# Performance work log

Measured on AMD Instinct MI355X. Metric: run time of the kernel, lower is better.

## Reference

```python
import jax, jax.numpy as jnp
import numpy as np

INPUT_DIM = 512
OUTPUT_DIM = 512
NUM_BASIS = 16
GRID_MIN, GRID_MAX = -2.0, 2.0
LN_EPS = 1e-5


def rbf_basis(x):
    # x: [batch, input_dim] -> [batch, input_dim, num_basis]
    centers = jnp.linspace(GRID_MIN, GRID_MAX, NUM_BASIS, dtype=x.dtype)  # [K]
    h = (GRID_MAX - GRID_MIN) / (NUM_BASIS - 1)
    z = (x[..., None] - centers) / h
    return jnp.exp(-(z * z))


def setup_inputs() -> dict:
    key = jax.random.key(0)
    k1, k2, k3 = jax.random.split(key, 3)
    x = jax.random.normal(k1, (4096, INPUT_DIM), dtype=jnp.float32)
    weights = jax.random.normal(k2, (OUTPUT_DIM, INPUT_DIM, NUM_BASIS), dtype=jnp.float32) * 0.1
    base_weights = jax.random.normal(k3, (OUTPUT_DIM, INPUT_DIM), dtype=jnp.float32) * 0.1
    ln_gamma = jnp.ones((OUTPUT_DIM,), dtype=jnp.float32)
    ln_beta = jnp.zeros((OUTPUT_DIM,), dtype=jnp.float32)
    return {"x": x, "weights": weights, "base_weights": base_weights,
            "ln_gamma": ln_gamma, "ln_beta": ln_beta}


def reference(x, weights, base_weights, ln_gamma, ln_beta):
    # per-edge basis expansion: [B, I, K]
    basis = rbf_basis(x)
    # fused contraction replacing the nested python loops:
    # out[b, j] = sum_{i,k} basis[b, i, k] * weights[j, i, k]
    out = jnp.einsum('bik,jik->bj', basis, weights)
    # residual base activation path
    out = out + jax.nn.silu(x) @ base_weights.T
    # layer norm over output_dim
    mean = jnp.mean(out, axis=-1, keepdims=True)
    var = jnp.var(out, axis=-1, keepdims=True)
    out = (out - mean) * jax.lax.rsqrt(var + LN_EPS) * ln_gamma + ln_beta
    return out
```

## Files before the change

### kernel.cpp

```cpp
#include <hip/hip_runtime.h>
#include <hip/hip_bf16.h>


typedef __bf16 bf16x8 __attribute__((ext_vector_type(8)));
typedef __bf16 bf16x4 __attribute__((ext_vector_type(4)));
typedef float  f32x4  __attribute__((ext_vector_type(4)));

#define KT 8704
#define SPLITS 8
#define KS (KT / SPLITS)
#define NIT (KS / 32)
#define CPE (4096 * 512)
#define ABUF (256 * 32)

__device__ __forceinline__ void gll16(const __bf16* g, __bf16* l) {
    __builtin_amdgcn_global_load_lds(
        (const __attribute__((address_space(1))) void*)g,
        (__attribute__((address_space(3))) void*)l, 16, 0, 0);
}

__global__ void prep_AB(const float* __restrict__ x, const float* __restrict__ W,
                        const float* __restrict__ Wb, __bf16* __restrict__ A,
                        __bf16* __restrict__ B) {
    if (blockIdx.x < 8192) {
        int t = blockIdx.x * 256 + threadIdx.x;
        int b = t >> 9;
        int i = t & 511;
        float xv = x[t];
        float zb = 3.75f * xv + 7.5f;
        bf16x8 lo, hi;
#pragma unroll
        for (int k = 0; k < 8; ++k) { float z = zb - (float)k; lo[k]   = (__bf16)__expf(-z * z); }
#pragma unroll
        for (int k = 8; k < 16; ++k){ float z = zb - (float)k; hi[k-8] = (__bf16)__expf(-z * z); }
        size_t base = (size_t)b * KT + (size_t)i * 16;
        *(bf16x8*)(A + base)     = lo;
        *(bf16x8*)(A + base + 8) = hi;
        float s = xv / (1.0f + __expf(-xv));
        A[(size_t)b * KT + 8192 + i] = (__bf16)s;
    } else {
        int t = (blockIdx.x - 8192) * 256 + threadIdx.x;
        int j = t / 2176;
        int c = (t - j * 2176) * 4;
        float4 v;
        if (c < 8192) v = *(const float4*)&W[(size_t)j * 8192 + c];
        else          v = *(const float4*)&Wb[(size_t)j * 512 + (c - 8192)];
        bf16x4 o;
        o[0] = (__bf16)v.x; o[1] = (__bf16)v.y; o[2] = (__bf16)v.z; o[3] = (__bf16)v.w;
        *(bf16x4*)&B[(size_t)j * KT + c] = o;
    }
}

__global__ __launch_bounds__(512, 2) void gemm_bt(const __bf16* __restrict__ A,
                                                  const __bf16* __restrict__ B,
                                                  __bf16* __restrict__ Cp) {
    __shared__ __attribute__((aligned(16))) __bf16 As[3 * ABUF];
    __shared__ __attribute__((aligned(16))) __bf16 Bs[3 * ABUF];

    const int tid  = threadIdx.x;
    const int wave = tid >> 6, lane = tid & 63;
    const int q    = lane >> 4, r16 = lane & 15;
    const int m0 = blockIdx.x * 256, n0 = blockIdx.y * 256, k0 = blockIdx.z * KS;
    const int wm = wave >> 2, wn = wave & 3;

    const int srow = tid >> 2, sqk = (tid & 3) ^ ((srow >> 1) & 3);
    const __bf16* gA0 = A + (size_t)(m0 + srow) * KT + k0 + sqk * 8;
    const __bf16* gA1 = A + (size_t)(m0 + srow + 128) * KT + k0 + sqk * 8;
    const __bf16* gB0 = B + (size_t)(n0 + srow) * KT + k0 + sqk * 8;
    const __bf16* gB1 = B + (size_t)(n0 + srow + 128) * KT + k0 + sqk * 8;

    f32x4 acc[8][4] = {};

    const int qa    = q ^ ((r16 >> 1) & 3);
    const int awOff = (wm * 128 + r16) * 32 + qa * 8;
    const int bwOff = (wn * 64  + r16) * 32 + qa * 8;

    auto stage = [&](int t, int sb) {
        const int ko = t * 32;
        const int so = sb * ABUF;
        gll16(gA0 + ko, &As[so + tid * 8]);
        gll16(gA1 + ko, &As[so + (tid + 512) * 8]);
        gll16(gB0 + ko, &Bs[so + tid * 8]);
        gll16(gB1 + ko, &Bs[so + (tid + 512) * 8]);
    };

    auto compute = [&](int cb) {
        const __bf16* Aw = &As[cb * ABUF + awOff];
        const __bf16* Bw = &Bs[cb * ABUF + bwOff];
        bf16x8 af[8], bg[4];
#pragma unroll
        for (int mi = 0; mi < 8; ++mi) af[mi] = *(const bf16x8*)(Aw + mi * 512);
#pragma unroll
        for (int ni = 0; ni < 4; ++ni) bg[ni] = *(const bf16x8*)(Bw + ni * 512);
        __builtin_amdgcn_s_setprio(1);
#pragma unroll
        for (int mi = 0; mi < 8; ++mi)
#pragma unroll
            for (int ni = 0; ni < 4; ++ni)
                acc[mi][ni] = __builtin_amdgcn_mfma_f32_16x16x32_bf16(
                    af[mi], bg[ni], acc[mi][ni], 0, 0, 0);
        __builtin_amdgcn_s_setprio(0);
    };

    stage(0, 0);
    stage(1, 1);
    asm volatile("s_waitcnt vmcnt(4)" ::: "memory");
    __builtin_amdgcn_s_barrier();

    int cb = 0;
    for (int it = 0; it < NIT - 1; ++it) {
        int sb = cb - 1; if (sb < 0) sb = 2;
        stage(it + 2, sb);
        compute(cb);
        asm volatile("s_waitcnt vmcnt(4)" ::: "memory");
        __builtin_amdgcn_s_barrier();
        cb = (cb == 2) ? 0 : cb + 1;
    }
    compute(cb);

    __bf16* Cb = Cp + (size_t)blockIdx.z * CPE;
#pragma unroll
    for (int mi = 0; mi < 8; ++mi) {
        const int row = m0 + wm * 128 + mi * 16 + q * 4;
#pragma unroll
        for (int ni = 0; ni < 4; ++ni) {
            const int col = n0 + wn * 64 + ni * 16 + r16;
#pragma unroll
            for (int r = 0; r < 4; ++r)
                Cb[(size_t)(row + r) * 512 + col] = (__bf16)acc[mi][ni][r];
        }
    }
}

__global__ void ln_kernel(const __bf16* __restrict__ Cp, const float* __restrict__ gamma,
                          const float* __restrict__ beta, float* __restrict__ out) {
    const int tid  = threadIdx.x;
    const int wave = tid >> 6, lane = tid & 63;
    const int row  = blockIdx.x * 4 + wave;
    const size_t base = (size_t)row * 512 + lane * 8;

    float v[8] = {};
    float s = 0.f, s2 = 0.f;
#pragma unroll
    for (int z = 0; z < SPLITS; ++z) {
        bf16x8 p = *(const bf16x8*)(Cp + (size_t)z * CPE + base);
#pragma unroll
        for (int j = 0; j < 8; ++j) v[j] += (float)p[j];
    }
#pragma unroll
    for (int j = 0; j < 8; ++j) { s += v[j]; s2 += v[j] * v[j]; }
#pragma unroll
    for (int m = 32; m >= 1; m >>= 1) {
        s  += __shfl_xor(s, m);
        s2 += __shfl_xor(s2, m);
    }
    const float mean = s * (1.0f / 512.0f);
    const float var  = s2 * (1.0f / 512.0f) - mean * mean;
    const float rs   = rsqrtf(var + 1e-5f);
    float4 o0, o1;
    const float4 g0 = *(const float4*)&gamma[lane * 8];
    const float4 g1 = *(const float4*)&gamma[lane * 8 + 4];
    const float4 b0 = *(const float4*)&beta[lane * 8];
    const float4 b1 = *(const float4*)&beta[lane * 8 + 4];
    o0.x = (v[0] - mean) * rs * g0.x + b0.x;
    o0.y = (v[1] - mean) * rs * g0.y + b0.y;
    o0.z = (v[2] - mean) * rs * g0.z + b0.z;
    o0.w = (v[3] - mean) * rs * g0.w + b0.w;
    o1.x = (v[4] - mean) * rs * g1.x + b1.x;
    o1.y = (v[5] - mean) * rs * g1.y + b1.y;
    o1.z = (v[6] - mean) * rs * g1.z + b1.z;
    o1.w = (v[7] - mean) * rs * g1.w + b1.w;
    *(float4*)&out[base]     = o0;
    *(float4*)&out[base + 4] = o1;
}

extern "C" void kernel_launch(void* const* d_in, const int* in_sizes, int n_in,
                              void* d_out, int out_size, void* d_ws, size_t ws_size,
                              hipStream_t stream) {
    const float* x     = (const float*)d_in[0];
    const float* W     = (const float*)d_in[1];
    const float* Wb    = (const float*)d_in[2];
    const float* gamma = (const float*)d_in[3];
    const float* beta  = (const float*)d_in[4];
    float* out = (float*)d_out;

    char* ws = (char*)d_ws;
    __bf16* A  = (__bf16*)ws;
    __bf16* Bm = (__bf16*)(ws + 71303168);
    __bf16* Cp = (__bf16*)(ws + 80216064);

    prep_AB<<<8192 + 4352, 256, 0, stream>>>(x, W, Wb, A, Bm);
    dim3 g(16, 2, SPLITS);
    gemm_bt<<<g, 512, 0, stream>>>(A, Bm, Cp);
    ln_kernel<<<1024, 256, 0, stream>>>(Cp, gamma, beta, out);
}
```

Measured before the change: 150.7 us.

## Restructure split-K GEMM main loop into 64-wide K tiles with phased prefetch

The GEMM now stages 64-wide K tiles in a double-buffered LDS layout, replacing the triple-buffered 32-wide tiles, with a new XOR swizzle. Each iteration runs four MFMA phases. Between phases it issues slices of the next tile's global-to-LDS loads, separated by barriers and raised scheduling priority. The aim is to overlap loads with matrix math more evenly and halve the per-K-step loop and barrier overhead. In exchange it adds more barriers per iteration, roughly 128KB of LDS, and the final iteration issues prefetches past the block's K slice.

```diff
diff --git a/kernel.cpp b/kernel.cpp
--- a/kernel.cpp
+++ b/kernel.cpp
@@ -9,9 +9,9 @@
 #define KT 8704
 #define SPLITS 8
 #define KS (KT / SPLITS)
-#define NIT (KS / 32)
+#define NT2 (KS / 64)
 #define CPE (4096 * 512)
-#define ABUF (256 * 32)
+#define ATILE (256 * 64)
 
 __device__ __forceinline__ void gll16(const __bf16* g, __bf16* l) {
     __builtin_amdgcn_global_load_lds(
@@ -54,8 +54,8 @@
 __global__ __launch_bounds__(512, 2) void gemm_bt(const __bf16* __restrict__ A,
                                                   const __bf16* __restrict__ B,
                                                   __bf16* __restrict__ Cp) {
-    __shared__ __attribute__((aligned(16))) __bf16 As[3 * ABUF];
-    __shared__ __attribute__((aligned(16))) __bf16 Bs[3 * ABUF];
+    __shared__ __attribute__((aligned(16))) __bf16 As[2 * ATILE];
+    __shared__ __attribute__((aligned(16))) __bf16 Bs[2 * ATILE];
 
     const int tid  = threadIdx.x;
     const int wave = tid >> 6, lane = tid & 63;
@@ -63,60 +63,115 @@
     const int m0 = blockIdx.x * 256, n0 = blockIdx.y * 256, k0 = blockIdx.z * KS;
     const int wm = wave >> 2, wn = wave & 3;
 
-    const int srow = tid >> 2, sqk = (tid & 3) ^ ((srow >> 1) & 3);
-    const __bf16* gA0 = A + (size_t)(m0 + srow) * KT + k0 + sqk * 8;
-    const __bf16* gA1 = A + (size_t)(m0 + srow + 128) * KT + k0 + sqk * 8;
-    const __bf16* gB0 = B + (size_t)(n0 + srow) * KT + k0 + sqk * 8;
-    const __bf16* gB1 = B + (size_t)(n0 + srow + 128) * KT + k0 + sqk * 8;
+    const int sr = tid >> 3;
+    const int sc = (tid & 7) ^ ((tid >> 4) & 7);
+    const __bf16* gA0 = A + (size_t)(m0 + sr) * KT       + k0 + sc * 8;
+    const __bf16* gA1 = A + (size_t)(m0 + 64  + sr) * KT + k0 + sc * 8;
+    const __bf16* gA2 = A + (size_t)(m0 + 128 + sr) * KT + k0 + sc * 8;
+    const __bf16* gA3 = A + (size_t)(m0 + 192 + sr) * KT + k0 + sc * 8;
+    const __bf16* gB0 = B + (size_t)(n0 + sr) * KT       + k0 + sc * 8;
+    const __bf16* gB1 = B + (size_t)(n0 + 64  + sr) * KT + k0 + sc * 8;
+    const __bf16* gB2 = B + (size_t)(n0 + 128 + sr) * KT + k0 + sc * 8;
+    const __bf16* gB3 = B + (size_t)(n0 + 192 + sr) * KT + k0 + sc * 8;
 
     f32x4 acc[8][4] = {};
 
-    const int qa    = q ^ ((r16 >> 1) & 3);
-    const int awOff = (wm * 128 + r16) * 32 + qa * 8;
-    const int bwOff = (wn * 64  + r16) * 32 + qa * 8;
-
-    auto stage = [&](int t, int sb) {
-        const int ko = t * 32;
-        const int so = sb * ABUF;
-        gll16(gA0 + ko, &As[so + tid * 8]);
-        gll16(gA1 + ko, &As[so + (tid + 512) * 8]);
-        gll16(gB0 + ko, &Bs[so + tid * 8]);
-        gll16(gB1 + ko, &Bs[so + (tid + 512) * 8]);
-    };
-
-    auto compute = [&](int cb) {
-        const __bf16* Aw = &As[cb * ABUF + awOff];
-        const __bf16* Bw = &Bs[cb * ABUF + bwOff];
-        bf16x8 af[8], bg[4];
-#pragma unroll
-        for (int mi = 0; mi < 8; ++mi) af[mi] = *(const bf16x8*)(Aw + mi * 512);
-#pragma unroll
-        for (int ni = 0; ni < 4; ++ni) bg[ni] = *(const bf16x8*)(Bw + ni * 512);
-        __builtin_amdgcn_s_setprio(1);
-#pragma unroll
-        for (int mi = 0; mi < 8; ++mi)
-#pragma unroll
-            for (int ni = 0; ni < 4; ++ni)
-                acc[mi][ni] = __builtin_amdgcn_mfma_f32_16x16x32_bf16(
-                    af[mi], bg[ni], acc[mi][ni], 0, 0, 0);
-        __builtin_amdgcn_s_setprio(0);
-    };
-
-    stage(0, 0);
-    stage(1, 1);
-    asm volatile("s_waitcnt vmcnt(4)" ::: "memory");
+    const int swl = (r16 >> 1) & 7;
+    const int qx0 = ((q)     ^ swl) * 8;
+    const int qx1 = ((4 + q) ^ swl) * 8;
+    const int aro = (wm * 128 + r16) * 64;
+    const int bro = (wn * 64  + r16) * 64;
+
+    gll16(gA0, &As[(size_t)tid * 8]);
+    gll16(gA1, &As[(size_t)(512 + tid) * 8]);
+    gll16(gA2, &As[(size_t)(1024 + tid) * 8]);
+    gll16(gA3, &As[(size_t)(1536 + tid) * 8]);
+    gll16(gB0, &Bs[(size_t)tid * 8]);
+    gll16(gB1, &Bs[(size_t)(512 + tid) * 8]);
+    gll16(gB2, &Bs[(size_t)(1024 + tid) * 8]);
+    gll16(gB3, &Bs[(size_t)(1536 + tid) * 8]);
+    gll16(gA0 + 64, &As[(size_t)(ATILE + tid * 8)]);
+    gll16(gA2 + 64, &As[(size_t)(ATILE + (1024 + tid) * 8)]);
+    asm volatile("s_waitcnt vmcnt(2)" ::: "memory");
     __builtin_amdgcn_s_barrier();
 
-    int cb = 0;
-    for (int it = 0; it < NIT - 1; ++it) {
-        int sb = cb - 1; if (sb < 0) sb = 2;
-        stage(it + 2, sb);
-        compute(cb);
-        asm volatile("s_waitcnt vmcnt(4)" ::: "memory");
-        __builtin_amdgcn_s_barrier();
-        cb = (cb == 2) ? 0 : cb + 1;
-    }
-    compute(cb);
+    bf16x8 a[4], b[4];
+    for (int u = 0; u < NT2; ++u) {
+        const int s   = u & 1;
+        const int cbo = s * ATILE;
+        const int so1 = (s ^ 1) * ATILE;
+        const int k1  = (u + 1) * 64;
+        const int k2  = (u + 2) * 64;
+
+#pragma unroll
+        for (int mi = 0; mi < 4; ++mi) a[mi] = *(const bf16x8*)(As + cbo + aro + mi * 1024 + qx0);
+#pragma unroll
+        for (int ni = 0; ni < 4; ++ni) b[ni] = *(const bf16x8*)(Bs + cbo + bro + ni * 1024 + qx0);
+        gll16(gB0 + k1, &Bs[(size_t)(so1 + tid * 8)]);
+        gll16(gB1 + k1, &Bs[(size_t)(so1 + (512 + tid) * 8)]);
+        __builtin_amdgcn_s_barrier();
+        asm volatile("s_waitcnt lgkmcnt(0)" ::: "memory");
+        __builtin_amdgcn_sched_barrier(0);
+        __builtin_amdgcn_s_setprio(1);
+#pragma unroll
+        for (int mi = 0; mi < 4; ++mi)
+#pragma unroll
+            for (int ni = 0; ni < 4; ++ni)
+                acc[mi][ni] = __builtin_amdgcn_mfma_f32_16x16x32_bf16(a[mi], b[ni], acc[mi][ni], 0, 0, 0);
+        __builtin_amdgcn_s_setprio(0);
+        __builtin_amdgcn_s_barrier();
+
+#pragma unroll
+        for (int mi = 0; mi < 4; ++mi) a[mi] = *(const bf16x8*)(As + cbo + aro + (4 + mi) * 1024 + qx0);
+        gll16(gB2 + k1, &Bs[(size_t)(so1 + (1024 + tid) * 8)]);
+        gll16(gB3 + k1, &Bs[(size_t)(so1 + (1536 + tid) * 8)]);
+        __builtin_amdgcn_s_barrier();
+        asm volatile("s_waitcnt lgkmcnt(0)" ::: "memory");
+        __builtin_amdgcn_sched_barrier(0);
+        __builtin_amdgcn_s_setprio(1);
+#pragma unroll
+        for (int mi = 0; mi < 4; ++mi)
+#pragma unroll
+            for (int ni = 0; ni < 4; ++ni)
+                acc[4 + mi][ni] = __builtin_amdgcn_mfma_f32_16x16x32_bf16(a[mi], b[ni], acc[4 + mi][ni], 0, 0, 0);
+        __builtin_amdgcn_s_setprio(0);
+        __builtin_amdgcn_s_barrier();
+
+#pragma unroll
+        for (int mi = 0; mi < 4; ++mi) a[mi] = *(const bf16x8*)(As + cbo + aro + mi * 1024 + qx1);
+#pragma unroll
+        for (int ni = 0; ni < 4; ++ni) b[ni] = *(const bf16x8*)(Bs + cbo + bro + ni * 1024 + qx1);
+        gll16(gA1 + k1, &As[(size_t)(so1 + (512 + tid) * 8)]);
+        gll16(gA3 + k1, &As[(size_t)(so1 + (1536 + tid) * 8)]);
+        __builtin_amdgcn_s_barrier();
+        asm volatile("s_waitcnt lgkmcnt(0)" ::: "memory");
+        __builtin_amdgcn_sched_barrier(0);
+        __builtin_amdgcn_s_setprio(1);
+#pragma unroll
+        for (int mi = 0; mi < 4; ++mi)
+#pragma unroll
+            for (int ni = 0; ni < 4; ++ni)
+                acc[mi][ni] = __builtin_amdgcn_mfma_f32_16x16x32_bf16(a[mi], b[ni], acc[mi][ni], 0, 0, 0);
+        __builtin_amdgcn_s_setprio(0);
+        __builtin_amdgcn_s_barrier();
+
+#pragma unroll
+        for (int mi = 0; mi < 4; ++mi) a[mi] = *(const bf16x8*)(As + cbo + aro + (4 + mi) * 1024 + qx1);
+        gll16(gA0 + k2, &As[(size_t)(cbo + tid * 8)]);
+        gll16(gA2 + k2, &As[(size_t)(cbo + (1024 + tid) * 8)]);
+        __builtin_amdgcn_s_barrier();
+        asm volatile("s_waitcnt lgkmcnt(0)" ::: "memory");
+        __builtin_amdgcn_sched_barrier(0);
+        __builtin_amdgcn_s_setprio(1);
+#pragma unroll
+        for (int mi = 0; mi < 4; ++mi)
+#pragma unroll
+            for (int ni = 0; ni < 4; ++ni)
+                acc[4 + mi][ni] = __builtin_amdgcn_mfma_f32_16x16x32_bf16(a[mi], b[ni], acc[4 + mi][ni], 0, 0, 0);
+        __builtin_amdgcn_s_setprio(0);
+        asm volatile("s_waitcnt vmcnt(2)" ::: "memory");
+        __builtin_amdgcn_s_barrier();
+    }
 
     __bf16* Cb = Cp + (size_t)blockIdx.z * CPE;
 #pragma unroll
```

Result: faster. 141.7 us (-6.0%).
